# Optimization experiments

Hardware: AMD Instinct MI355X
Metric: run time of the kernel (lower is better)

## Reference

```python
import jax, jax.numpy as jnp
from jax import lax
import numpy as np

IGNORE_INDEX = -100


def setup_inputs() -> dict:
    key = jax.random.key(0)
    k1, k2, k3 = jax.random.split(key, 3)
    N, D, V = 8192, 2048, 32000
    x = jax.random.normal(k1, (N, D), dtype=jnp.float32) * (D ** -0.5)
    proj_weight = jax.random.normal(k2, (V, D), dtype=jnp.float32) * (D ** -0.5)
    target = jax.random.randint(k3, (N,), 0, V, dtype=jnp.int64 if jax.config.jax_enable_x64 else jnp.int32)
    return {"x": x, "proj_weight": proj_weight, "target": target, "num_splits": 4}


def reference(x, proj_weight, target, num_splits):
    # Fused linear-projection + cross-entropy, chunked over the token dim so the
    # full [N, V] logits tensor is never materialized (only [N/num_splits, V]).
    N, D = x.shape
    chunk = N // num_splits  # N chosen divisible by num_splits
    x_c = x.reshape(num_splits, chunk, D)
    t_c = target.reshape(num_splits, chunk)

    def body(carry, inp):
        loss_sum, count = carry
        xi, ti = inp  # [chunk, D], [chunk]
        logits = jnp.einsum('nd,vd->nv', xi, proj_weight)  # [chunk, V]
        lse = jax.nn.logsumexp(logits, axis=-1)            # [chunk]
        valid = ti != IGNORE_INDEX
        safe_t = jnp.where(valid, ti, 0)
        tgt_logit = jnp.take_along_axis(logits, safe_t[:, None], axis=-1)[:, 0]
        loss = jnp.where(valid, lse - tgt_logit, 0.0)
        return (loss_sum + loss.sum(), count + valid.sum()), None

    init = (jnp.float32(0.0), jnp.int32(0))
    (loss_sum, count), _ = lax.scan(body, init, (x_c, t_c))
    return loss_sum / count.astype(jnp.float32)  # mean over non-ignored tokens
```

## Files before the change

kernel.cpp:

```cpp
#include <hip/hip_runtime.h>
#include <hip/hip_bf16.h>


typedef __bf16 bf16_t;
typedef bf16_t bf16x8 __attribute__((ext_vector_type(8)));
typedef float f32x4 __attribute__((ext_vector_type(4)));

constexpr int N_TOK = 8192;
constexpr int DIM   = 2048;
constexpr int VOCAB = 32000;
constexpr int BM = 128, BN = 128, BK = 64;
constexpr int MT  = N_TOK / BM;
constexpr int NVT = VOCAB / BN;
constexpr int IGNORE_INDEX = -100;

#define GPTR(p) ((const __attribute__((address_space(1))) void*)(p))
#define LPTR(p) ((__attribute__((address_space(3))) void*)(p))

__device__ __forceinline__ bf16_t f2bf(float f) {
  union { float f; unsigned u; } in; in.f = f;
  unsigned u = in.u;
  unsigned r = u + 0x7fffu + ((u >> 16) & 1u);
  union { unsigned short s; bf16_t b; } out;
  out.s = (unsigned short)(r >> 16);
  return out.b;
}

__global__ __launch_bounds__(256) void cvt_f32_bf16(const float* __restrict__ src,
                                                    bf16_t* __restrict__ dst, int n8) {
  int i = blockIdx.x * 256 + threadIdx.x;
  if (i >= n8) return;
  const float4* s = (const float4*)src;
  float4 a = s[2 * (size_t)i], b = s[2 * (size_t)i + 1];
  bf16x8 o;
  o[0] = f2bf(a.x); o[1] = f2bf(a.y); o[2] = f2bf(a.z); o[3] = f2bf(a.w);
  o[4] = f2bf(b.x); o[5] = f2bf(b.y); o[6] = f2bf(b.z); o[7] = f2bf(b.w);
  *(bf16x8*)(dst + (size_t)i * 8) = o;
}

__global__ __launch_bounds__(256, 2) void fused_gemm_lse(
    const bf16_t* __restrict__ X, const bf16_t* __restrict__ W,
    const int* __restrict__ target,
    float2* __restrict__ partials, float* __restrict__ tgt_logit) {
  __shared__ __align__(16) char smem[2 * BM * BK * 2];
  bf16_t* As = (bf16_t*)smem;
  bf16_t* Bs = (bf16_t*)(smem + BM * BK * 2);

  const int tid  = threadIdx.x;
  const int lane = tid & 63;
  const int wid  = tid >> 6;
  const int wr   = wid >> 1;
  const int wc   = wid & 1;
  const int l15  = lane & 15;
  const int lg   = lane >> 4;

  int bid  = blockIdx.x;
  int wgid = (bid & 7) * 2000 + (bid >> 3);
  int mt = wgid & (MT - 1);
  int vt = wgid >> 6;
  const int brow = mt * BM;
  const int bcol = vt * BN;

  f32x4 acc[4][4];
#pragma unroll
  for (int m = 0; m < 4; ++m)
#pragma unroll
    for (int n = 0; n < 4; ++n)
      acc[m][n] = (f32x4){0.f, 0.f, 0.f, 0.f};

  for (int kt = 0; kt < DIM; kt += BK) {
#pragma unroll
    for (int it = 0; it < 4; ++it) {
      int c   = it * 256 + tid;
      int row = c >> 3;
      int cin = c & 7;
      int sc  = cin ^ (row & 7);
      const bf16_t* ga = X + (size_t)(brow + row) * DIM + kt + sc * 8;
      const bf16_t* gb = W + (size_t)(bcol + row) * DIM + kt + sc * 8;
      __builtin_amdgcn_global_load_lds(GPTR(ga), LPTR(As + c * 8), 16, 0, 0);
      __builtin_amdgcn_global_load_lds(GPTR(gb), LPTR(Bs + c * 8), 16, 0, 0);
    }
    __syncthreads();
#pragma unroll
    for (int ks = 0; ks < 2; ++ks) {
      bf16x8 a[4], b[4];
#pragma unroll
      for (int m = 0; m < 4; ++m) {
        int row = wr * 64 + m * 16 + l15;
        int ch  = (ks * 4 + lg) ^ (row & 7);
        a[m] = *(const bf16x8*)(As + row * BK + ch * 8);
      }
#pragma unroll
      for (int n = 0; n < 4; ++n) {
        int row = wc * 64 + n * 16 + l15;
        int ch  = (ks * 4 + lg) ^ (row & 7);
        b[n] = *(const bf16x8*)(Bs + row * BK + ch * 8);
      }
#pragma unroll
      for (int m = 0; m < 4; ++m)
#pragma unroll
        for (int n = 0; n < 4; ++n)
          acc[m][n] = __builtin_amdgcn_mfma_f32_16x16x32_bf16(a[m], b[n], acc[m][n], 0, 0, 0);
    }
    __syncthreads();
  }

  float* smax = (float*)smem;
  float* ssum = (float*)(smem + 1024);
#pragma unroll
  for (int m = 0; m < 4; ++m) {
#pragma unroll
    for (int i = 0; i < 4; ++i) {
      int rloc = wr * 64 + m * 16 + lg * 4 + i;
      int grow = brow + rloc;
      int tgt  = target[grow];
      float v0 = acc[m][0][i], v1 = acc[m][1][i], v2 = acc[m][2][i], v3 = acc[m][3][i];
      int colbase = bcol + wc * 64 + l15;
      if (colbase      == tgt) tgt_logit[grow] = v0;
      if (colbase + 16 == tgt) tgt_logit[grow] = v1;
      if (colbase + 32 == tgt) tgt_logit[grow] = v2;
      if (colbase + 48 == tgt) tgt_logit[grow] = v3;
      float rmax = fmaxf(fmaxf(v0, v1), fmaxf(v2, v3));
#pragma unroll
      for (int s = 1; s < 16; s <<= 1) rmax = fmaxf(rmax, __shfl_xor(rmax, s));
      float rsum = __expf(v0 - rmax) + __expf(v1 - rmax) +
                   __expf(v2 - rmax) + __expf(v3 - rmax);
#pragma unroll
      for (int s = 1; s < 16; s <<= 1) rsum += __shfl_xor(rsum, s);
      if (l15 == 0) { smax[rloc * 2 + wc] = rmax; ssum[rloc * 2 + wc] = rsum; }
    }
  }
  __syncthreads();
  if (tid < BM) {
    float m0 = smax[tid * 2], m1 = smax[tid * 2 + 1];
    float s0 = ssum[tid * 2], s1 = ssum[tid * 2 + 1];
    float M = fmaxf(m0, m1);
    float S = s0 * __expf(m0 - M) + s1 * __expf(m1 - M);
    partials[(size_t)(brow + tid) * NVT + vt] = make_float2(M, S);
  }
}

__global__ __launch_bounds__(256) void finalize_rows(
    const float2* __restrict__ partials, const float* __restrict__ tgt_logit,
    const int* __restrict__ target, float2* __restrict__ blocksum) {
  int tid = threadIdx.x, lane = tid & 63, w = tid >> 6;
  int row = blockIdx.x * 4 + w;
  float M = -1e30f, S = 0.f;
  for (int i = lane; i < NVT; i += 64) {
    float2 p = partials[(size_t)row * NVT + i];
    float Mn = fmaxf(M, p.x);
    S = S * __expf(M - Mn) + p.y * __expf(p.x - Mn);
    M = Mn;
  }
#pragma unroll
  for (int s = 1; s < 64; s <<= 1) {
    float Mo = __shfl_xor(M, s), So = __shfl_xor(S, s);
    float Mn = fmaxf(M, Mo);
    S = S * __expf(M - Mn) + So * __expf(Mo - Mn);
    M = Mn;
  }
  __shared__ float ls[4], cs[4];
  if (lane == 0) {
    int t = target[row];
    bool valid = (t != IGNORE_INDEX);
    float lse = M + __logf(S);
    ls[w] = valid ? (lse - tgt_logit[row]) : 0.f;
    cs[w] = valid ? 1.f : 0.f;
  }
  __syncthreads();
  if (tid == 0)
    blocksum[blockIdx.x] = make_float2(ls[0] + ls[1] + ls[2] + ls[3],
                                       cs[0] + cs[1] + cs[2] + cs[3]);
}

__global__ __launch_bounds__(256) void finalize_out(
    const float2* __restrict__ blocksum, float* __restrict__ out) {
  int tid = threadIdx.x;
  float s = 0.f, c = 0.f;
  for (int i = tid; i < N_TOK / 4; i += 256) {
    float2 b = blocksum[i];
    s += b.x; c += b.y;
  }
#pragma unroll
  for (int k = 1; k < 64; k <<= 1) { s += __shfl_xor(s, k); c += __shfl_xor(c, k); }
  __shared__ float ss[4], cc[4];
  int w = tid >> 6;
  if ((tid & 63) == 0) { ss[w] = s; cc[w] = c; }
  __syncthreads();
  if (tid == 0) out[0] = (ss[0] + ss[1] + ss[2] + ss[3]) / (cc[0] + cc[1] + cc[2] + cc[3]);
}

extern "C" void kernel_launch(void* const* d_in, const int* in_sizes, int n_in,
                              void* d_out, int out_size, void* d_ws, size_t ws_size,
                              hipStream_t stream) {
  const float* x = (const float*)d_in[0];
  const float* w = (const float*)d_in[1];
  const int* target = (const int*)d_in[2];
  float* out = (float*)d_out;

  char* ws = (char*)d_ws;
  size_t off = 0;
  bf16_t* Xbf = (bf16_t*)(ws + off); off += (size_t)N_TOK * DIM * 2;
  bf16_t* Wbf = (bf16_t*)(ws + off); off += (size_t)VOCAB * DIM * 2;
  float2* partials = (float2*)(ws + off); off += (size_t)N_TOK * NVT * 8;
  float*  tgtlog   = (float*)(ws + off);  off += (size_t)N_TOK * 4;
  float2* blocksum = (float2*)(ws + off); off += (size_t)(N_TOK / 4) * 8;
  (void)ws_size; (void)in_sizes; (void)n_in; (void)out_size;

  cvt_f32_bf16<<<(N_TOK * DIM / 8) / 256, 256, 0, stream>>>(x, Xbf, N_TOK * DIM / 8);
  cvt_f32_bf16<<<(VOCAB * DIM / 8) / 256, 256, 0, stream>>>(w, Wbf, VOCAB * DIM / 8);
  fused_gemm_lse<<<MT * NVT, 256, 0, stream>>>(Xbf, Wbf, target, partials, tgtlog);
  finalize_rows<<<N_TOK / 4, 256, 0, stream>>>(partials, tgtlog, target, blocksum);
  finalize_out<<<1, 256, 0, stream>>>(blocksum, out);
}
```

Before: 1.557 ms.

## Use 256x256 tiles with double-buffered LDS pipelining and merged conversion kernel

The GEMM moves from 128x128 tiles with 256 threads and a single LDS buffer to 256x256 tiles with 512 threads. It uses two 64KB LDS buffers, prefetching the next K tile in quarter pieces interleaved with MFMA phases, with setprio and explicit vmcnt waits. The aim is to hide global-load latency and raise arithmetic intensity per tile. The LSE epilogue now merges four column-warp partials. The two fp32-to-bf16 conversion launches are fused into one. The 128KB of LDS limits occupancy to one block per CU and raises register pressure.

```diff
diff --git a/kernel.cpp b/kernel.cpp
--- a/kernel.cpp
+++ b/kernel.cpp
@@ -9,9 +9,10 @@
 constexpr int N_TOK = 8192;
 constexpr int DIM   = 2048;
 constexpr int VOCAB = 32000;
-constexpr int BM = 128, BN = 128, BK = 64;
+constexpr int BM = 256, BN = 256, BK = 64;
 constexpr int MT  = N_TOK / BM;
 constexpr int NVT = VOCAB / BN;
+constexpr int NKT = DIM / BK;
 constexpr int IGNORE_INDEX = -100;
 
 #define GPTR(p) ((const __attribute__((address_space(1))) void*)(p))
@@ -26,92 +27,174 @@
   return out.b;
 }
 
-__global__ __launch_bounds__(256) void cvt_f32_bf16(const float* __restrict__ src,
-                                                    bf16_t* __restrict__ dst, int n8) {
+constexpr int XN8 = N_TOK * DIM / 8;
+constexpr int WN8 = VOCAB * DIM / 8;
+
+__global__ __launch_bounds__(256) void cvt_both(const float* __restrict__ x,
+                                                const float* __restrict__ w,
+                                                bf16_t* __restrict__ xb,
+                                                bf16_t* __restrict__ wb) {
   int i = blockIdx.x * 256 + threadIdx.x;
-  if (i >= n8) return;
+  const float* src; bf16_t* dst; int j;
+  if (i < XN8) { src = x; dst = xb; j = i; }
+  else { j = i - XN8; if (j >= WN8) return; src = w; dst = wb; }
   const float4* s = (const float4*)src;
-  float4 a = s[2 * (size_t)i], b = s[2 * (size_t)i + 1];
+  float4 a = s[2 * (size_t)j], b = s[2 * (size_t)j + 1];
   bf16x8 o;
   o[0] = f2bf(a.x); o[1] = f2bf(a.y); o[2] = f2bf(a.z); o[3] = f2bf(a.w);
   o[4] = f2bf(b.x); o[5] = f2bf(b.y); o[6] = f2bf(b.z); o[7] = f2bf(b.w);
-  *(bf16x8*)(dst + (size_t)i * 8) = o;
-}
-
-__global__ __launch_bounds__(256, 2) void fused_gemm_lse(
+  *(bf16x8*)(dst + (size_t)j * 8) = o;
+}
+
+__global__ __launch_bounds__(512, 2) void fused_gemm_lse(
     const bf16_t* __restrict__ X, const bf16_t* __restrict__ W,
     const int* __restrict__ target,
     float2* __restrict__ partials, float* __restrict__ tgt_logit) {
-  __shared__ __align__(16) char smem[2 * BM * BK * 2];
-  bf16_t* As = (bf16_t*)smem;
-  bf16_t* Bs = (bf16_t*)(smem + BM * BK * 2);
+  __shared__ __align__(16) char smem[131072];
 
   const int tid  = threadIdx.x;
   const int lane = tid & 63;
   const int wid  = tid >> 6;
-  const int wr   = wid >> 1;
-  const int wc   = wid & 1;
+  const int wr   = wid >> 2;
+  const int wc   = wid & 3;
   const int l15  = lane & 15;
   const int lg   = lane >> 4;
 
   int bid  = blockIdx.x;
-  int wgid = (bid & 7) * 2000 + (bid >> 3);
+  int wgid = (bid & 7) * (MT * NVT / 8) + (bid >> 3);
   int mt = wgid & (MT - 1);
-  int vt = wgid >> 6;
+  int vt = wgid >> 5;
   const int brow = mt * BM;
   const int bcol = vt * BN;
 
-  f32x4 acc[4][4];
-#pragma unroll
-  for (int m = 0; m < 4; ++m)
+  const bf16_t* Abase = X + (size_t)brow * DIM;
+  const bf16_t* Bbase = W + (size_t)bcol * DIM;
+
+  auto stage = [&](const bf16_t* rowbase, int ktile, int ldsoff) {
+#pragma unroll
+    for (int i = 0; i < 2; ++i) {
+      int c = i * 512 + tid;
+      int row = c >> 3, cin = c & 7;
+      int sc = cin ^ (row & 7);
+      const bf16_t* g = rowbase + (size_t)row * DIM + ktile * BK + sc * 8;
+      __builtin_amdgcn_global_load_lds(GPTR(g), LPTR(smem + ldsoff + c * 16), 16, 0, 0);
+    }
+  };
+  auto ldA = [&](int slot, int row, int ks) -> bf16x8 {
+    int ch = (ks * 4 + lg) ^ (row & 7);
+    return *(const bf16x8*)(smem + slot + row * 128 + ch * 16);
+  };
+  auto ldB = [&](int slot, int row, int ks) -> bf16x8 {
+    int ch = (ks * 4 + lg) ^ (row & 7);
+    return *(const bf16x8*)(smem + slot + 32768 + row * 128 + ch * 16);
+  };
+
+  f32x4 acc[8][4];
+#pragma unroll
+  for (int m = 0; m < 8; ++m)
 #pragma unroll
     for (int n = 0; n < 4; ++n)
       acc[m][n] = (f32x4){0.f, 0.f, 0.f, 0.f};
 
-  for (int kt = 0; kt < DIM; kt += BK) {
-#pragma unroll
-    for (int it = 0; it < 4; ++it) {
-      int c   = it * 256 + tid;
-      int row = c >> 3;
-      int cin = c & 7;
-      int sc  = cin ^ (row & 7);
-      const bf16_t* ga = X + (size_t)(brow + row) * DIM + kt + sc * 8;
-      const bf16_t* gb = W + (size_t)(bcol + row) * DIM + kt + sc * 8;
-      __builtin_amdgcn_global_load_lds(GPTR(ga), LPTR(As + c * 8), 16, 0, 0);
-      __builtin_amdgcn_global_load_lds(GPTR(gb), LPTR(Bs + c * 8), 16, 0, 0);
-    }
-    __syncthreads();
-#pragma unroll
-    for (int ks = 0; ks < 2; ++ks) {
-      bf16x8 a[4], b[4];
-#pragma unroll
-      for (int m = 0; m < 4; ++m) {
-        int row = wr * 64 + m * 16 + l15;
-        int ch  = (ks * 4 + lg) ^ (row & 7);
-        a[m] = *(const bf16x8*)(As + row * BK + ch * 8);
-      }
-#pragma unroll
-      for (int n = 0; n < 4; ++n) {
-        int row = wc * 64 + n * 16 + l15;
-        int ch  = (ks * 4 + lg) ^ (row & 7);
-        b[n] = *(const bf16x8*)(Bs + row * BK + ch * 8);
-      }
-#pragma unroll
-      for (int m = 0; m < 4; ++m)
-#pragma unroll
-        for (int n = 0; n < 4; ++n)
-          acc[m][n] = __builtin_amdgcn_mfma_f32_16x16x32_bf16(a[m], b[n], acc[m][n], 0, 0, 0);
-    }
-    __syncthreads();
-  }
-
+  stage(Abase,             0, 0);
+  stage(Abase + 128 * DIM, 0, 16384);
+  stage(Bbase,             0, 32768);
+  stage(Bbase + 128 * DIM, 0, 49152);
+  stage(Abase,             1, 65536);
+  stage(Abase + 128 * DIM, 1, 65536 + 16384);
+  asm volatile("s_waitcnt vmcnt(4)" ::: "memory");
+  __builtin_amdgcn_s_barrier();
+
+  for (int t = 0; t < NKT; ++t) {
+    const int cur = (t & 1) * 65536;
+    const int nxt = 65536 - cur;
+    const int ktB = (t + 1) & (NKT - 1);
+    const int ktA = (t + 2) & (NKT - 1);
+
+    bf16x8 a0[4][2], a1[4][2], b[4][2];
+
+#pragma unroll
+    for (int m = 0; m < 4; ++m)
+#pragma unroll
+      for (int ks = 0; ks < 2; ++ks)
+        a0[m][ks] = ldA(cur, wr * 128 + m * 16 + l15, ks);
+#pragma unroll
+    for (int n = 0; n < 2; ++n)
+#pragma unroll
+      for (int ks = 0; ks < 2; ++ks)
+        b[n][ks] = ldB(cur, wc * 64 + n * 16 + l15, ks);
+    stage(Bbase, ktB, nxt + 32768);
+    __builtin_amdgcn_s_barrier();
+    __builtin_amdgcn_s_setprio(1);
+#pragma unroll
+    for (int m = 0; m < 4; ++m)
+#pragma unroll
+      for (int n = 0; n < 2; ++n)
+#pragma unroll
+        for (int ks = 0; ks < 2; ++ks)
+          acc[m][n] = __builtin_amdgcn_mfma_f32_16x16x32_bf16(a0[m][ks], b[n][ks], acc[m][n], 0, 0, 0);
+    __builtin_amdgcn_s_setprio(0);
+    __builtin_amdgcn_s_barrier();
+
+#pragma unroll
+    for (int m = 0; m < 4; ++m)
+#pragma unroll
+      for (int ks = 0; ks < 2; ++ks)
+        a1[m][ks] = ldA(cur, wr * 128 + 64 + m * 16 + l15, ks);
+#pragma unroll
+    for (int n = 2; n < 4; ++n)
+#pragma unroll
+      for (int ks = 0; ks < 2; ++ks)
+        b[n][ks] = ldB(cur, wc * 64 + n * 16 + l15, ks);
+    stage(Bbase + 128 * DIM, ktB, nxt + 49152);
+    __builtin_amdgcn_s_barrier();
+    __builtin_amdgcn_s_setprio(1);
+#pragma unroll
+    for (int m = 0; m < 4; ++m)
+#pragma unroll
+      for (int n = 2; n < 4; ++n)
+#pragma unroll
+        for (int ks = 0; ks < 2; ++ks)
+          acc[m][n] = __builtin_amdgcn_mfma_f32_16x16x32_bf16(a0[m][ks], b[n][ks], acc[m][n], 0, 0, 0);
+    __builtin_amdgcn_s_setprio(0);
+    __builtin_amdgcn_s_barrier();
+
+    stage(Abase, ktA, cur);
+    __builtin_amdgcn_s_barrier();
+    __builtin_amdgcn_s_setprio(1);
+#pragma unroll
+    for (int m = 0; m < 4; ++m)
+#pragma unroll
+      for (int n = 2; n < 4; ++n)
+#pragma unroll
+        for (int ks = 0; ks < 2; ++ks)
+          acc[m + 4][n] = __builtin_amdgcn_mfma_f32_16x16x32_bf16(a1[m][ks], b[n][ks], acc[m + 4][n], 0, 0, 0);
+    __builtin_amdgcn_s_setprio(0);
+    __builtin_amdgcn_s_barrier();
+
+    stage(Abase + 128 * DIM, ktA, cur + 16384);
+    __builtin_amdgcn_s_barrier();
+    __builtin_amdgcn_s_setprio(1);
+#pragma unroll
+    for (int m = 0; m < 4; ++m)
+#pragma unroll
+      for (int n = 0; n < 2; ++n)
+#pragma unroll
+        for (int ks = 0; ks < 2; ++ks)
+          acc[m + 4][n] = __builtin_amdgcn_mfma_f32_16x16x32_bf16(a1[m][ks], b[n][ks], acc[m + 4][n], 0, 0, 0);
+    __builtin_amdgcn_s_setprio(0);
+    asm volatile("s_waitcnt vmcnt(4)" ::: "memory");
+    __builtin_amdgcn_s_barrier();
+  }
+
+  __syncthreads();
   float* smax = (float*)smem;
-  float* ssum = (float*)(smem + 1024);
-#pragma unroll
-  for (int m = 0; m < 4; ++m) {
+  float* ssum = (float*)(smem + 4096);
+#pragma unroll
+  for (int m = 0; m < 8; ++m) {
 #pragma unroll
     for (int i = 0; i < 4; ++i) {
-      int rloc = wr * 64 + m * 16 + lg * 4 + i;
+      int rloc = wr * 128 + m * 16 + lg * 4 + i;
       int grow = brow + rloc;
       int tgt  = target[grow];
       float v0 = acc[m][0][i], v1 = acc[m][1][i], v2 = acc[m][2][i], v3 = acc[m][3][i];
@@ -127,15 +210,19 @@
                    __expf(v2 - rmax) + __expf(v3 - rmax);
 #pragma unroll
       for (int s = 1; s < 16; s <<= 1) rsum += __shfl_xor(rsum, s);
-      if (l15 == 0) { smax[rloc * 2 + wc] = rmax; ssum[rloc * 2 + wc] = rsum; }
+      if (l15 == 0) { smax[rloc * 4 + wc] = rmax; ssum[rloc * 4 + wc] = rsum; }
     }
   }
   __syncthreads();
   if (tid < BM) {
-    float m0 = smax[tid * 2], m1 = smax[tid * 2 + 1];
-    float s0 = ssum[tid * 2], s1 = ssum[tid * 2 + 1];
-    float M = fmaxf(m0, m1);
-    float S = s0 * __expf(m0 - M) + s1 * __expf(m1 - M);
+    float M = smax[tid * 4], S = ssum[tid * 4];
+#pragma unroll
+    for (int c = 1; c < 4; ++c) {
+      float m2 = smax[tid * 4 + c], s2 = ssum[tid * 4 + c];
+      float Mn = fmaxf(M, m2);
+      S = S * __expf(M - Mn) + s2 * __expf(m2 - Mn);
+      M = Mn;
+    }
     partials[(size_t)(brow + tid) * NVT + vt] = make_float2(M, S);
   }
 }
@@ -207,9 +294,9 @@
   float2* blocksum = (float2*)(ws + off); off += (size_t)(N_TOK / 4) * 8;
   (void)ws_size; (void)in_sizes; (void)n_in; (void)out_size;
 
-  cvt_f32_bf16<<<(N_TOK * DIM / 8) / 256, 256, 0, stream>>>(x, Xbf, N_TOK * DIM / 8);
-  cvt_f32_bf16<<<(VOCAB * DIM / 8) / 256, 256, 0, stream>>>(w, Wbf, VOCAB * DIM / 8);
-  fused_gemm_lse<<<MT * NVT, 256, 0, stream>>>(Xbf, Wbf, target, partials, tgtlog);
+  int cvt_blocks = (XN8 + WN8 + 255) / 256;
+  cvt_both<<<cvt_blocks, 256, 0, stream>>>(x, w, Xbf, Wbf);
+  fused_gemm_lse<<<MT * NVT, 512, 0, stream>>>(Xbf, Wbf, target, partials, tgtlog);
   finalize_rows<<<N_TOK / 4, 256, 0, stream>>>(partials, tgtlog, target, blocksum);
   finalize_out<<<1, 256, 0, stream>>>(blocksum, out);
 }
```

Result: faster. 1.508 ms (-3.1%).
